# Kernel optimization log

Hardware: AMD Instinct MI355X
Metric: run time of the kernel (lower is better)

## Reference

```python
import jax, jax.numpy as jnp
import numpy as np

N_QUBITS = 12
BATCH = 2048
N_CLASSES = 10


def build_tape(n):
    # 2 layers of: RX on all wires (id 0), RY (id 1), RZ (id 2), then a CRX ring
    # (id 4 forward in layer 0, id 5 reversed in layer 1). 96 gates total for n=12.
    tape = []
    for layer in range(2):
        for i in range(n):
            tape.append(("rx", (i,)))
        for i in range(n):
            tape.append(("ry", (i,)))
        for i in range(n):
            tape.append(("rz", (i,)))
        order = range(n) if layer == 0 else range(n - 1, -1, -1)
        for i in order:
            tape.append(("crx", (i, (i + 1) % n)))
    return tape


def rx_mat(t):
    c = jnp.cos(t / 2).astype(jnp.complex64)
    s = jnp.sin(t / 2).astype(jnp.complex64)
    return jnp.stack([jnp.stack([c, -1j * s]), jnp.stack([-1j * s, c])])


def ry_mat(t):
    c = jnp.cos(t / 2).astype(jnp.complex64)
    s = jnp.sin(t / 2).astype(jnp.complex64)
    return jnp.stack([jnp.stack([c, -s]), jnp.stack([s, c])])


def rz_mat(t):
    em = jnp.exp(-1j * t.astype(jnp.complex64) / 2)
    ep = jnp.exp(1j * t.astype(jnp.complex64) / 2)
    z = jnp.zeros((), jnp.complex64)
    return jnp.stack([jnp.stack([em, z]), jnp.stack([z, ep])])


def apply_1q(psi, U, w):
    # psi: [B] + [2]*n, gate on wire w (axis 1+w)
    psi = jnp.moveaxis(psi, 1 + w, -1)
    psi = psi @ U.T
    return jnp.moveaxis(psi, -1, 1 + w)


def apply_crx(psi, theta, c, t):
    a_c, a_t = 1 + c, 1 + t
    psi = jnp.moveaxis(psi, a_c, 1)  # control -> axis 1
    if a_t < a_c:
        a_t += 1
    psi = jnp.moveaxis(psi, a_t, -1)  # target -> last axis
    U = rx_mat(theta)
    p1 = psi[:, 1] @ U.T  # apply RX only on control=1 branch
    psi = jnp.stack([psi[:, 0], p1], axis=1)
    psi = jnp.moveaxis(psi, -1, a_t)
    return jnp.moveaxis(psi, 1, a_c)


def expvals(psi, n):
    # <X_i>, <Y_i>, <Z_i> for each qubit; returns [B, 3n] ordered X..Y..Z (PL order)
    xs, ys, zs = [], [], []
    for i in range(n):
        p = jnp.moveaxis(psi, 1 + i, -1).reshape(psi.shape[0], -1, 2)
        z = jnp.sum(jnp.abs(p[..., 0]) ** 2 - jnp.abs(p[..., 1]) ** 2, axis=1)
        cross = jnp.sum(jnp.conj(p[..., 0]) * p[..., 1], axis=1)
        xs.append(2.0 * jnp.real(cross))
        ys.append(2.0 * jnp.imag(cross))
        zs.append(jnp.real(z))
    return jnp.stack(xs + ys + zs, axis=1).astype(jnp.float32)


def setup_inputs() -> dict:
    key = jax.random.key(0)
    k0, k1, k2 = jax.random.split(key, 3)
    sv = jax.random.normal(k0, (BATCH, 2 ** N_QUBITS), dtype=jnp.float32)
    sv = sv / jnp.linalg.norm(sv, axis=1, keepdims=True)  # valid quantum states
    n_gates = len(build_tape(N_QUBITS))
    angles = jax.random.normal(k1, (n_gates,), dtype=jnp.float32)
    W = jax.random.normal(k2, (N_CLASSES, 3 * N_QUBITS), dtype=jnp.float32) * 0.1
    b = jnp.zeros((N_CLASSES,), jnp.float32)
    return {"state_vectors": sv, "angles": angles, "W": W, "b": b}


def reference(state_vectors, angles, W, b):
    tape = build_tape(N_QUBITS)
    psi = state_vectors.astype(jnp.complex64).reshape((-1,) + (2,) * N_QUBITS)
    for g, (kind, wires) in enumerate(tape):
        th = angles[g]
        if kind == "rx":
            psi = apply_1q(psi, rx_mat(th), wires[0])
        elif kind == "ry":
            psi = apply_1q(psi, ry_mat(th), wires[0])
        elif kind == "rz":
            psi = apply_1q(psi, rz_mat(th), wires[0])
        else:
            psi = apply_crx(psi, th, wires[0], wires[1])
    feats = expvals(psi, N_QUBITS)  # [B, 3*n_qubits]
    return feats @ W.T + b
```

## Files before the change

kernel.cpp:

```cpp
#include <hip/hip_runtime.h>

#define DIM 4096
using F2 = float2;


__device__ __forceinline__ int addrA(int r, int t) { return (r << 7) | t; }
__device__ __forceinline__ int addrB(int r, int t) { return ((t >> 3) << 8) | (r << 3) | (t & 7); }
__device__ __forceinline__ int addrC(int r, int t) { return ((r & 1) << 11) | (t << 4) | (r >> 1); }
__device__ __forceinline__ int swzAB(int a) { return a ^ ((a >> 5) & 8); }
__device__ __forceinline__ int swzBC(int a) { return a ^ ((a >> 4) & 15) ^ ((a >> 5) & 8); }

__device__ __forceinline__ F2 pk_mul_bl(F2 a, F2 u) {
    F2 d;
    asm("v_pk_mul_f32 %0, %1, %2 op_sel:[0,0] op_sel_hi:[1,0]"
        : "=v"(d) : "v"(a), "v"(u));
    return d;
}
__device__ __forceinline__ void pk_cross(F2& d, F2 a, F2 u) {
    asm("v_pk_fma_f32 %0, %1, %2, %0 op_sel:[1,1,0] op_sel_hi:[0,1,1] neg_lo:[1,0,0]"
        : "+v"(d) : "v"(a), "v"(u));
}
__device__ __forceinline__ void pk_fma_bl(F2& d, F2 a, F2 u) {
    asm("v_pk_fma_f32 %0, %1, %2, %0 op_sel:[0,0,0] op_sel_hi:[1,0,1]"
        : "+v"(d) : "v"(a), "v"(u));
}
__device__ __forceinline__ void pk_swapneg(F2& d, F2 a, F2 cs) {
    asm("v_pk_fma_f32 %0, %1, %2, %0 op_sel:[1,1,0] op_sel_hi:[0,1,1] neg_hi:[1,0,0]"
        : "+v"(d) : "v"(a), "v"(cs));
}
__device__ __forceinline__ void pk_fma(F2& d, F2 a, F2 b) {
    asm("v_pk_fma_f32 %0, %1, %2, %0" : "+v"(d) : "v"(a), "v"(b));
}
__device__ __forceinline__ void pk_imacc(F2& d, F2 a0, F2 a1) {
    asm("v_pk_fma_f32 %0, %1, %2, %0 op_sel:[0,1,0] op_sel_hi:[1,0,1] neg_hi:[1,0,0]"
        : "+v"(d) : "v"(a0), "v"(a1));
}
__device__ __forceinline__ F2 pk_cmul(F2 u, F2 a) {
    F2 d = pk_mul_bl(a, u);
    pk_cross(d, a, u);
    return d;
}
__device__ __forceinline__ void pk_cfma(F2& d, F2 u, F2 a) {
    pk_fma_bl(d, a, u);
    pk_cross(d, a, u);
}

__device__ __forceinline__ void build_u(float tx, float ty, float tz, float* u) {
    float sx = sinf(0.5f*tx), cx = cosf(0.5f*tx);
    float sy = sinf(0.5f*ty), cy = cosf(0.5f*ty);
    float sz = sinf(0.5f*tz), cz = cosf(0.5f*tz);
    float A00r = cy*cx, A00i =  sy*sx;
    float A01r = -sy*cx, A01i = -cy*sx;
    float A10r =  sy*cx, A10i = -cy*sx;
    float A11r =  cy*cx, A11i = -sy*sx;
    u[0] = cz*A00r + sz*A00i;  u[1] = cz*A00i - sz*A00r;
    u[2] = cz*A01r + sz*A01i;  u[3] = cz*A01i - sz*A01r;
    u[4] = cz*A10r - sz*A10i;  u[5] = cz*A10i + sz*A10r;
    u[6] = cz*A11r - sz*A11i;  u[7] = cz*A11i + sz*A11r;
}

__global__ void prep_kernel(const float* __restrict__ ang, float* __restrict__ coef) {
    int t = threadIdx.x;
    if (t < 12) {
        float u[8]; build_u(ang[t], ang[12+t], ang[24+t], u);
#pragma unroll
        for (int j = 0; j < 8; ++j) coef[t*8 + j] = u[j];
    } else if (t < 24) {
        int q = t - 12;
        float u[8]; build_u(ang[48+q], ang[60+q], ang[72+q], u);
#pragma unroll
        for (int j = 0; j < 8; ++j) coef[192 + q*8 + j] = u[j];
    } else if (t < 36) {
        int c = t - 24;
        float th = 0.5f * ang[95 - c];
        coef[296 + c*2]     = cosf(th);
        coef[296 + c*2 + 1] = sinf(th);
    } else if (t < 47) {
        int q = t - 35;
        float u[8]; build_u(ang[q], ang[12+q], ang[24+q], u);
        float c = cosf(0.5f*ang[36+q-1]), s = sinf(0.5f*ang[36+q-1]);
        float m[8];
        m[0] = c*u[0] + s*u[5];  m[1] = c*u[1] - s*u[4];
        m[2] = c*u[2] + s*u[7];  m[3] = c*u[3] - s*u[6];
        m[4] = s*u[1] + c*u[4];  m[5] = -s*u[0] + c*u[5];
        m[6] = s*u[3] + c*u[6];  m[7] = -s*u[2] + c*u[7];
#pragma unroll
        for (int j = 0; j < 8; ++j) coef[96 + q*8 + j] = m[j];
    } else if (t == 47) {
        float u[8]; build_u(ang[48], ang[60], ang[72], u);
        float c = cosf(0.5f*ang[47]), s = sinf(0.5f*ang[47]);
        float m[8];
        m[0] = c*u[0] + s*u[3];  m[1] = c*u[1] - s*u[2];
        m[2] = s*u[1] + c*u[2];  m[3] = -s*u[0] + c*u[3];
        m[4] = c*u[4] + s*u[7];  m[5] = c*u[5] - s*u[6];
        m[6] = s*u[5] + c*u[6];  m[7] = -s*u[4] + c*u[7];
#pragma unroll
        for (int j = 0; j < 8; ++j) coef[288 + j] = m[j];
    }
}

template<int M>
__device__ __forceinline__ void g1q(F2* amp, const float* __restrict__ u) {
    F2 u00 = {u[0], u[1]}, u01 = {u[2], u[3]};
    F2 u10 = {u[4], u[5]}, u11 = {u[6], u[7]};
#pragma unroll
    for (int r0 = 0; r0 < 32; ++r0) {
        if (r0 & M) continue;
        const int r1 = r0 + M;
        F2 a0 = amp[r0], a1 = amp[r1];
        F2 n0 = pk_cmul(u00, a0); pk_cfma(n0, u01, a1);
        F2 n1 = pk_cmul(u10, a0); pk_cfma(n1, u11, a1);
        amp[r0] = n0; amp[r1] = n1;
    }
}

template<int MSEL, int M>
__device__ __forceinline__ void fg1q(F2* amp, const float* __restrict__ uA,
                                     const float* __restrict__ uB) {
    F2 a00 = {uA[0], uA[1]}, a01 = {uA[2], uA[3]}, a10 = {uA[4], uA[5]}, a11 = {uA[6], uA[7]};
    F2 b00 = {uB[0], uB[1]}, b01 = {uB[2], uB[3]}, b10 = {uB[4], uB[5]}, b11 = {uB[6], uB[7]};
#pragma unroll
    for (int r0 = 0; r0 < 32; ++r0) {
        if (r0 & M) continue;
        const int r1 = r0 + M;
        const bool sel = (r0 & MSEL) != 0;
        F2 u00 = sel ? b00 : a00, u01 = sel ? b01 : a01;
        F2 u10 = sel ? b10 : a10, u11 = sel ? b11 : a11;
        F2 a0 = amp[r0], a1 = amp[r1];
        F2 n0 = pk_cmul(u00, a0); pk_cfma(n0, u01, a1);
        F2 n1 = pk_cmul(u10, a0); pk_cfma(n1, u11, a1);
        amp[r0] = n0; amp[r1] = n1;
    }
}

template<int MC, int MT>
__device__ __forceinline__ void crx(F2* amp, F2 cs) {
#pragma unroll
    for (int r0 = 0; r0 < 32; ++r0) {
        if (!(r0 & MC) || (r0 & MT)) continue;
        const int r1 = r0 + MT;
        F2 a0 = amp[r0], a1 = amp[r1];
        F2 n0 = pk_mul_bl(a0, cs); pk_swapneg(n0, a1, cs);
        F2 n1 = pk_mul_bl(a1, cs); pk_swapneg(n1, a0, cs);
        amp[r0] = n0; amp[r1] = n1;
    }
}

template<int M>
__device__ __forceinline__ void expv(const F2* amp, int q, int lane,
                                     float& fx, float& fy, float& fz) {
    F2 zp = {0.f, 0.f}, zm = {0.f, 0.f}, xp = {0.f, 0.f}, ip = {0.f, 0.f};
#pragma unroll
    for (int r0 = 0; r0 < 32; ++r0) {
        if (r0 & M) continue;
        const int r1 = r0 + M;
        F2 a0 = amp[r0], a1 = amp[r1];
        pk_fma(zp, a0, a0);
        pk_fma(zm, a1, a1);
        pk_fma(xp, a0, a1);
        pk_imacc(ip, a0, a1);
    }
    float zz = (zp.x + zp.y) - (zm.x + zm.y);
    float xr = 2.f * (xp.x + xp.y);
    float xi = 2.f * (ip.x + ip.y);
#pragma unroll
    for (int off = 32; off; off >>= 1) {
        xr += __shfl_xor(xr, off);
        xi += __shfl_xor(xi, off);
        zz += __shfl_xor(zz, off);
    }
    if (lane == q) { fx = xr; fy = xi; fz = zz; }
}

#define ST(ADDR, SWZ) \
  { _Pragma("unroll") for (int r = 0; r < 32; ++r) psi[SWZ(ADDR(r, t))] = amp[r]; }
#define LDP(ADDR, SWZ, M) \
  { _Pragma("unroll") for (int k = 0; k < 32; ++k) { \
      const int j = k >> 1; \
      const int r0 = ((j & ~((M) - 1)) << 1) | (j & ((M) - 1)); \
      const int r = (k & 1) ? (r0 + (M)) : r0; \
      amp[r] = psi[SWZ(ADDR(r, t))]; } }

#define U0P(q, M)       g1q<M>(amp, cf + (q)*8)
#define FU0(q, MS, M)   fg1q<MS, M>(amp, cf + (q)*8, cf + 96 + (q)*8)
#define U1P(q, M)       g1q<M>(amp, cf + 192 + (q)*8)
#define FU1_0()         fg1q<2, 1>(amp, cf + 192, cf + 288)
#define CR1(c, MC, MT)  crx<MC, MT>(amp, F2{cf[296 + (c)*2], cf[296 + (c)*2 + 1]})
#define EXPV(q, M)      expv<M>(amp, q, lane, fx, fy, fz)

__global__ __launch_bounds__(128, 1)
void qsim_kernel(const float* __restrict__ sv,
                 const float* __restrict__ cf,
                 const float* __restrict__ W,
                 const float* __restrict__ bvec,
                 float* __restrict__ out)
{
    __shared__ F2 psi[DIM];
    const int t = threadIdx.x;
    const int b = blockIdx.x;
    const int lane = t & 63, w = t >> 6;

    F2 amp[32];
    const float* svb = sv + (size_t)b * DIM;
#pragma unroll
    for (int r = 0; r < 32; ++r)
        amp[r] = make_float2(svb[(r << 7) | t], 0.f);

    float fx = 0.f, fy = 0.f, fz = 0.f;

    U0P(0, 16);
    FU0(1, 16, 8); FU0(2, 8, 4); FU0(3, 4, 2); FU0(4, 2, 1);
    ST(addrA, swzAB);
    __syncthreads();
    LDP(addrB, swzAB, 8);
    __syncthreads();

    FU0(5, 16, 8); FU0(6, 8, 4); FU0(7, 4, 2); FU0(8, 2, 1);
    ST(addrB, swzBC);
    __syncthreads();
    LDP(addrC, swzBC, 8);
    __syncthreads();

    FU0(9, 16, 8); FU0(10, 8, 4); FU0(11, 4, 2);
    FU1_0();
    U1P(8, 16); U1P(9, 8); U1P(10, 4); U1P(11, 2);
    CR1(11, 2, 1); CR1(10, 4, 2); CR1(9, 8, 4); CR1(8, 16, 8);
    ST(addrC, swzBC);
    EXPV(9, 8); EXPV(10, 4); EXPV(11, 2);
    __syncthreads();
    LDP(addrB, swzBC, 16);
    __syncthreads();

    U1P(4, 16); U1P(5, 8); U1P(6, 4); U1P(7, 2);
    CR1(7, 2, 1); CR1(6, 4, 2); CR1(5, 8, 4); CR1(4, 16, 8);
    ST(addrB, swzAB);
    EXPV(5, 8); EXPV(6, 4); EXPV(7, 2); EXPV(8, 1);
    __syncthreads();
    LDP(addrA, swzAB, 8);
    __syncthreads();

    U1P(1, 8); U1P(2, 4); U1P(3, 2);
    CR1(3, 2, 1); CR1(2, 4, 2); CR1(1, 8, 4); CR1(0, 16, 8);
    EXPV(0, 16); EXPV(1, 8); EXPV(2, 4); EXPV(3, 2); EXPV(4, 1);

    float* fbuf = (float*)psi;
    if (lane < 12) {
        fbuf[w * 36 + lane]      = fx;
        fbuf[w * 36 + 12 + lane] = fy;
        fbuf[w * 36 + 24 + lane] = fz;
    }
    __syncthreads();
    if (t < 10) {
        float a = bvec[t];
#pragma unroll
        for (int f = 0; f < 36; ++f)
            a += W[t * 36 + f] * (fbuf[f] + fbuf[36 + f]);
        out[(size_t)b * 10 + t] = a;
    }
}

extern "C" void kernel_launch(void* const* d_in, const int* in_sizes, int n_in,
                              void* d_out, int out_size, void* d_ws, size_t ws_size,
                              hipStream_t stream) {
    const float* sv     = (const float*)d_in[0];
    const float* angles = (const float*)d_in[1];
    const float* W      = (const float*)d_in[2];
    const float* bvec   = (const float*)d_in[3];
    float* out  = (float*)d_out;
    float* coef = (float*)d_ws;
    int batch = in_sizes[0] / DIM;
    prep_kernel<<<1, 64, 0, stream>>>(angles, coef);
    qsim_kernel<<<batch, 128, 0, stream>>>(sv, coef, W, bvec, out);
}
```

Before: 134.1 us.

## Halve shared-memory footprint by transposing state in two halves with overlapped gates

```diff
diff --git a/kernel.cpp b/kernel.cpp
--- a/kernel.cpp
+++ b/kernel.cpp
@@ -4,11 +4,12 @@
 using F2 = float2;
 
 
-__device__ __forceinline__ int addrA(int r, int t) { return (r << 7) | t; }
-__device__ __forceinline__ int addrB(int r, int t) { return ((t >> 3) << 8) | (r << 3) | (t & 7); }
-__device__ __forceinline__ int addrC(int r, int t) { return ((r & 1) << 11) | (t << 4) | (r >> 1); }
-__device__ __forceinline__ int swzAB(int a) { return a ^ ((a >> 5) & 8); }
-__device__ __forceinline__ int swzBC(int a) { return a ^ ((a >> 4) & 15) ^ ((a >> 5) & 8); }
+__device__ __forceinline__ int caddrA (int r, int t) { return ((r >> 1) << 7) | t; }
+__device__ __forceinline__ int caddrB1(int r, int t) { return ((t >> 3) << 7) | ((r >> 1) << 3) | (t & 7); }
+__device__ __forceinline__ int caddrB2(int r, int t) { return ((t >> 3) << 7) | ((r & 1) << 6) | ((r >> 2) << 3) | (t & 7); }
+__device__ __forceinline__ int caddrC2(int r, int t) { return ((r & 1) << 10) | (t << 3) | (r >> 2); }
+__device__ __forceinline__ int s1(int a) { return a ^ ((a >> 5) & 8); }
+__device__ __forceinline__ int s2(int a) { return a ^ ((a >> 4) & 15); }
 
 __device__ __forceinline__ F2 pk_mul_bl(F2 a, F2 u) {
     F2 d;
@@ -99,13 +100,14 @@
     }
 }
 
-template<int M>
+template<int M, int SB, int HB>
 __device__ __forceinline__ void g1q(F2* amp, const float* __restrict__ u) {
     F2 u00 = {u[0], u[1]}, u01 = {u[2], u[3]};
     F2 u10 = {u[4], u[5]}, u11 = {u[6], u[7]};
 #pragma unroll
     for (int r0 = 0; r0 < 32; ++r0) {
         if (r0 & M) continue;
+        if (SB != 0 && (r0 & SB) != HB) continue;
         const int r1 = r0 + M;
         F2 a0 = amp[r0], a1 = amp[r1];
         F2 n0 = pk_cmul(u00, a0); pk_cfma(n0, u01, a1);
@@ -114,7 +116,7 @@
     }
 }
 
-template<int MSEL, int M>
+template<int MSEL, int M, int SB, int HB>
 __device__ __forceinline__ void fg1q(F2* amp, const float* __restrict__ uA,
                                      const float* __restrict__ uB) {
     F2 a00 = {uA[0], uA[1]}, a01 = {uA[2], uA[3]}, a10 = {uA[4], uA[5]}, a11 = {uA[6], uA[7]};
@@ -122,6 +124,7 @@
 #pragma unroll
     for (int r0 = 0; r0 < 32; ++r0) {
         if (r0 & M) continue;
+        if (SB != 0 && (r0 & SB) != HB) continue;
         const int r1 = r0 + M;
         const bool sel = (r0 & MSEL) != 0;
         F2 u00 = sel ? b00 : a00, u01 = sel ? b01 : a01;
@@ -172,21 +175,38 @@
     if (lane == q) { fx = xr; fy = xi; fz = zz; }
 }
 
-#define ST(ADDR, SWZ) \
-  { _Pragma("unroll") for (int r = 0; r < 32; ++r) psi[SWZ(ADDR(r, t))] = amp[r]; }
-#define LDP(ADDR, SWZ, M) \
-  { _Pragma("unroll") for (int k = 0; k < 32; ++k) { \
+template<int M, int SB>
+__device__ __forceinline__ int r0_of(int j, int hb) {
+    int r = hb ? SB : 0, b = 1;
+#pragma unroll
+    for (int p = 0; p < 5; ++p) {
+        const int mm = 1 << p;
+        if (mm == M || mm == SB) continue;
+        if (j & b) r |= mm;
+        b <<= 1;
+    }
+    return r;
+}
+
+#define ST_H(CADDR, SWZ, SB, HB) \
+  { _Pragma("unroll") for (int r = 0; r < 32; ++r) { \
+      if ((r & (SB)) != (HB)) continue; \
+      psi[SWZ(CADDR(r, t))] = amp[r]; } }
+#define LD_H(CADDR, SWZ, M, SB, HB) \
+  { _Pragma("unroll") for (int k = 0; k < 16; ++k) { \
       const int j = k >> 1; \
-      const int r0 = ((j & ~((M) - 1)) << 1) | (j & ((M) - 1)); \
+      const int r0 = r0_of<M, SB>(j, (HB) != 0); \
       const int r = (k & 1) ? (r0 + (M)) : r0; \
-      amp[r] = psi[SWZ(ADDR(r, t))]; } }
-
-#define U0P(q, M)       g1q<M>(amp, cf + (q)*8)
-#define FU0(q, MS, M)   fg1q<MS, M>(amp, cf + (q)*8, cf + 96 + (q)*8)
-#define U1P(q, M)       g1q<M>(amp, cf + 192 + (q)*8)
-#define FU1_0()         fg1q<2, 1>(amp, cf + 192, cf + 288)
-#define CR1(c, MC, MT)  crx<MC, MT>(amp, F2{cf[296 + (c)*2], cf[296 + (c)*2 + 1]})
-#define EXPV(q, M)      expv<M>(amp, q, lane, fx, fy, fz)
+      amp[r] = psi[SWZ(CADDR(r, t))]; } }
+
+#define U0P(q, M)               g1q<M, 0, 0>(amp, cf + (q)*8)
+#define FU0(q, MS, M)           fg1q<MS, M, 0, 0>(amp, cf + (q)*8, cf + 96 + (q)*8)
+#define FU0_H(q, MS, M, SB, HB) fg1q<MS, M, SB, HB>(amp, cf + (q)*8, cf + 96 + (q)*8)
+#define U1P(q, M)               g1q<M, 0, 0>(amp, cf + 192 + (q)*8)
+#define U1P_H(q, M, SB, HB)     g1q<M, SB, HB>(amp, cf + 192 + (q)*8)
+#define FU1_0()                 fg1q<4, 1, 0, 0>(amp, cf + 192, cf + 288)
+#define CR1(c, MC, MT)          crx<MC, MT>(amp, F2{cf[296 + (c)*2], cf[296 + (c)*2 + 1]})
+#define EXPV(q, M)              expv<M>(amp, q, lane, fx, fy, fz)
 
 __global__ __launch_bounds__(128, 1)
 void qsim_kernel(const float* __restrict__ sv,
@@ -195,7 +215,7 @@
                  const float* __restrict__ bvec,
                  float* __restrict__ out)
 {
-    __shared__ F2 psi[DIM];
+    __shared__ F2 psi[2048];
     const int t = threadIdx.x;
     const int b = blockIdx.x;
     const int lane = t & 63, w = t >> 6;
@@ -210,39 +230,67 @@
 
     U0P(0, 16);
     FU0(1, 16, 8); FU0(2, 8, 4); FU0(3, 4, 2); FU0(4, 2, 1);
-    ST(addrA, swzAB);
-    __syncthreads();
-    LDP(addrB, swzAB, 8);
-    __syncthreads();
-
-    FU0(5, 16, 8); FU0(6, 8, 4); FU0(7, 4, 2); FU0(8, 2, 1);
-    ST(addrB, swzBC);
-    __syncthreads();
-    LDP(addrC, swzBC, 8);
-    __syncthreads();
-
-    FU0(9, 16, 8); FU0(10, 8, 4); FU0(11, 4, 2);
+
+    ST_H(caddrA, s1, 1, 0);
+    __syncthreads();
+    LD_H(caddrB1, s1, 16, 1, 0);
+    __syncthreads();
+    ST_H(caddrA, s1, 1, 1);
+    FU0_H(5, 1, 16, 1, 0);
+    __syncthreads();
+    LD_H(caddrB1, s1, 16, 1, 1);
+    FU0_H(5, 1, 16, 1, 1);
+
+    FU0(6, 16, 8); FU0(7, 8, 4); FU0(8, 4, 2);
+
+    __syncthreads();
+    ST_H(caddrB2, s2, 2, 0);
+    __syncthreads();
+    LD_H(caddrC2, s2, 16, 2, 0);
+    __syncthreads();
+    ST_H(caddrB2, s2, 2, 2);
+    FU0_H(9, 2, 16, 2, 0);
+    __syncthreads();
+    LD_H(caddrC2, s2, 16, 2, 2);
+    FU0_H(9, 2, 16, 2, 2);
+
+    FU0(10, 16, 8); FU0(11, 8, 4);
     FU1_0();
-    U1P(8, 16); U1P(9, 8); U1P(10, 4); U1P(11, 2);
-    CR1(11, 2, 1); CR1(10, 4, 2); CR1(9, 8, 4); CR1(8, 16, 8);
-    ST(addrC, swzBC);
-    EXPV(9, 8); EXPV(10, 4); EXPV(11, 2);
-    __syncthreads();
-    LDP(addrB, swzBC, 16);
-    __syncthreads();
-
-    U1P(4, 16); U1P(5, 8); U1P(6, 4); U1P(7, 2);
-    CR1(7, 2, 1); CR1(6, 4, 2); CR1(5, 8, 4); CR1(4, 16, 8);
-    ST(addrB, swzAB);
-    EXPV(5, 8); EXPV(6, 4); EXPV(7, 2); EXPV(8, 1);
-    __syncthreads();
-    LDP(addrA, swzAB, 8);
-    __syncthreads();
-
-    U1P(1, 8); U1P(2, 4); U1P(3, 2);
+    U1P(8, 2); U1P(9, 16); U1P(10, 8); U1P(11, 4);
+    CR1(11, 4, 1); CR1(10, 8, 4); CR1(9, 16, 8); CR1(8, 2, 16);
+
+    __syncthreads();
+    ST_H(caddrC2, s2, 2, 0);
+    EXPV(9, 16); EXPV(10, 8); EXPV(11, 4);
+    __syncthreads();
+    LD_H(caddrB2, s2, 1, 2, 0);
+    __syncthreads();
+    ST_H(caddrC2, s2, 2, 2);
+    U1P_H(4, 1, 2, 0);
+    __syncthreads();
+    LD_H(caddrB2, s2, 1, 2, 2);
+    U1P_H(4, 1, 2, 2);
+
+    U1P(5, 16); U1P(6, 8); U1P(7, 4);
+    CR1(7, 4, 2); CR1(6, 8, 4); CR1(5, 16, 8); CR1(4, 1, 16);
+
+    __syncthreads();
+    ST_H(caddrB1, s1, 1, 0);
+    EXPV(5, 16); EXPV(6, 8); EXPV(7, 4); EXPV(8, 2);
+    __syncthreads();
+    LD_H(caddrA, s1, 8, 1, 0);
+    __syncthreads();
+    ST_H(caddrB1, s1, 1, 1);
+    U1P_H(1, 8, 1, 0);
+    __syncthreads();
+    LD_H(caddrA, s1, 8, 1, 1);
+    U1P_H(1, 8, 1, 1);
+
+    U1P(2, 4); U1P(3, 2);
     CR1(3, 2, 1); CR1(2, 4, 2); CR1(1, 8, 4); CR1(0, 16, 8);
     EXPV(0, 16); EXPV(1, 8); EXPV(2, 4); EXPV(3, 2); EXPV(4, 1);
 
+    __syncthreads();
     float* fbuf = (float*)psi;
     if (lane < 12) {
         fbuf[w * 36 + lane]      = fx;
```

Result: no change. 133.2 us (-0.7%).
